# Optimization experiments

Measured on AMD Instinct MI355X. Metric: run time of the kernel, lower is better.

## Reference

```python
import jax, jax.numpy as jnp
import numpy as np

B, C, N = 64, 81, 8732


def setup_inputs() -> dict:
    key = jax.random.key(0)
    k1, k2, k3, k4, k5 = jax.random.split(key, 5)
    ploc = jax.random.normal(k1, (B, 4, N), dtype=jnp.float32)
    plabel = jax.random.normal(k2, (B, C, N), dtype=jnp.float32)
    # gloc: uniform, shifted positive so gwh/dwh log is well-defined
    gloc = jax.random.uniform(k3, (B, 4, N), dtype=jnp.float32) * 0.9 + 0.05
    glabel = jax.random.randint(k4, (B, N), 0, C, dtype=jnp.int64)
    # default boxes: keep widths/heights bounded away from 0
    dboxes = jax.random.uniform(k5, (1, 4, N), dtype=jnp.float32) * 0.9 + 0.1
    return {"ploc": ploc, "plabel": plabel, "gloc": gloc, "glabel": glabel, "dboxes": dboxes}


def _smooth_l1(x):
    ax = jnp.abs(x)
    return jnp.where(ax < 1.0, 0.5 * ax * ax, ax - 0.5)


def reference(ploc, plabel, gloc, glabel, dboxes):
    mask = glabel > 0                       # [B, N] positive anchors
    num_pos = mask.sum(axis=1)              # [B]

    # encode ground-truth boxes as offsets relative to default boxes
    dxy, dwh = dboxes[:, :2, :], dboxes[:, 2:, :]
    gxy = (gloc[:, :2, :] - dxy) / dwh
    gwh = jnp.log(gloc[:, 2:, :] / dwh)
    goff = jnp.concatenate([gxy, gwh], axis=1)  # [B, 4, N]

    # localization loss: smooth L1 summed over coords, masked to positives
    loc = _smooth_l1(ploc - goff).sum(axis=1)   # [B, N]
    loc_loss = (mask * loc).sum(axis=1)         # [B]

    # per-anchor cross entropy
    logp = jax.nn.log_softmax(plabel, axis=1)   # [B, C, N]
    closs = -jnp.take_along_axis(logp, glabel[:, None, :], axis=1)[:, 0, :]  # [B, N]

    # hard negative mining via rank (double argsort, descending)
    con_neg = jnp.where(mask, 0.0, closs)
    con_idx = jnp.argsort(-con_neg, axis=1)
    con_rank = jnp.argsort(con_idx, axis=1)
    neg_num = jnp.minimum(3 * num_pos, N)[:, None]
    neg_mask = con_rank < neg_num
    con_loss = (closs * (mask.astype(jnp.float32) + neg_mask.astype(jnp.float32))).sum(axis=1)

    total = loc_loss + con_loss
    num_mask = (num_pos > 0).astype(jnp.float32)
    npos = jnp.clip(num_pos.astype(jnp.float32), 1e-6)
    return ((total * num_mask) / npos).mean()
```

## Files before the change

kernel.cpp:

```cpp
#include <hip/hip_runtime.h>
#include <math.h>

#define BATCH 64
#define NCLS  81
#define NANCH 8732
#define NG    (NANCH / 4)
#define BLK   256
#define BPB   ((NG + BLK - 1) / BLK)

struct Accum {
    float loc[BATCH];
    float posc[BATCH];
    float negc[BATCH];
    int   cnt[BATCH];
};

__device__ inline float smooth_l1(float d) {
    float a = fabsf(d);
    return (a < 1.f) ? 0.5f * a * a : a - 0.5f;
}

__global__ void k_init(Accum* __restrict__ acc, float* __restrict__ out) {
    unsigned int* w = (unsigned int*)acc;
    w[threadIdx.x] = 0u;
    if (threadIdx.x == 0) out[0] = 0.f;
}

__global__ __launch_bounds__(256) void k_main(
    const float* __restrict__ ploc, const float* __restrict__ plabel,
    const float* __restrict__ gloc, const int* __restrict__ glabel,
    const float* __restrict__ dboxes, Accum* __restrict__ acc)
{
    const int b   = blockIdx.x / BPB;
    const int gid = (blockIdx.x % BPB) * BLK + threadIdx.x;

    float l_loc = 0.f, l_posc = 0.f, l_negc = 0.f;
    int   l_cnt = 0;

    if (gid < NG) {
        const float4* pl4 = (const float4*)(plabel + (size_t)b * NCLS * NANCH);
        const int4*   gp  = (const int4*)(glabel + (size_t)b * NANCH);
        const int4    gi  = gp[gid];
        const int g[4] = {gi.x, gi.y, gi.z, gi.w};

        float m[4], s[4], xg[4];
#pragma unroll
        for (int i = 0; i < 4; ++i) { m[i] = -INFINITY; s[i] = 0.f; xg[i] = 0.f; }

        for (int c = 0; c < NCLS; ++c) {
            float4 xv = pl4[c * NG + gid];
            float x[4] = {xv.x, xv.y, xv.z, xv.w};
#pragma unroll
            for (int i = 0; i < 4; ++i) {
                float nm = fmaxf(m[i], x[i]);
                float e  = __expf(fminf(m[i], x[i]) - nm);
                s[i] = (x[i] > m[i]) ? s[i] * e + 1.f : s[i] + e;
                m[i] = nm;
                if (c == g[i]) xg[i] = x[i];
            }
        }

        const float4* pploc = (const float4*)(ploc + (size_t)b * 4 * NANCH);
        const float4* pgloc = (const float4*)(gloc + (size_t)b * 4 * NANCH);
        const float4* pdb   = (const float4*)dboxes;
        float P[4][4], G[4][4], D[4][4];
#pragma unroll
        for (int ch = 0; ch < 4; ++ch) {
            float4 p = pploc[ch * NG + gid];
            float4 q = pgloc[ch * NG + gid];
            float4 d = pdb[ch * NG + gid];
            P[ch][0]=p.x; P[ch][1]=p.y; P[ch][2]=p.z; P[ch][3]=p.w;
            G[ch][0]=q.x; G[ch][1]=q.y; G[ch][2]=q.z; G[ch][3]=q.w;
            D[ch][0]=d.x; D[ch][1]=d.y; D[ch][2]=d.z; D[ch][3]=d.w;
        }

#pragma unroll
        for (int i = 0; i < 4; ++i) {
            float gx = (G[0][i] - D[0][i]) / D[2][i];
            float gy = (G[1][i] - D[1][i]) / D[3][i];
            float gw = __logf(G[2][i] / D[2][i]);
            float gh = __logf(G[3][i] / D[3][i]);
            float loc_i = smooth_l1(P[0][i] - gx) + smooth_l1(P[1][i] - gy)
                        + smooth_l1(P[2][i] - gw) + smooth_l1(P[3][i] - gh);
            float closs = m[i] + __logf(s[i]) - xg[i];
            bool  mk = g[i] > 0;
            l_loc  += mk ? loc_i : 0.f;
            l_posc += mk ? closs : 0.f;
            l_negc += mk ? 0.f : closs;
            l_cnt  += mk ? 1 : 0;
        }
    }

#pragma unroll
    for (int off = 32; off; off >>= 1) {
        l_loc  += __shfl_down(l_loc, off);
        l_posc += __shfl_down(l_posc, off);
        l_negc += __shfl_down(l_negc, off);
        l_cnt  += __shfl_down(l_cnt, off);
    }
    __shared__ float sl[4], sp[4], sn[4];
    __shared__ int   sc[4];
    const int wave = threadIdx.x >> 6, lane = threadIdx.x & 63;
    if (lane == 0) { sl[wave] = l_loc; sp[wave] = l_posc; sn[wave] = l_negc; sc[wave] = l_cnt; }
    __syncthreads();
    if (threadIdx.x == 0) {
        float a = 0.f, p = 0.f, n = 0.f; int ct = 0;
#pragma unroll
        for (int w = 0; w < 4; ++w) { a += sl[w]; p += sp[w]; n += sn[w]; ct += sc[w]; }
        atomicAdd(&acc->loc[b],  a);
        atomicAdd(&acc->posc[b], p);
        atomicAdd(&acc->negc[b], n);
        atomicAdd(&acc->cnt[b],  ct);
    }
}

__device__ float closs_at(const float* __restrict__ plabel, int b, int n, int g) {
    const float* p = plabel + (size_t)b * NCLS * NANCH + n;
    float m = -INFINITY, s = 0.f, xg = 0.f;
    for (int c = 0; c < NCLS; ++c) {
        float x = p[(size_t)c * NANCH];
        float nm = fmaxf(m, x);
        float e  = __expf(fminf(m, x) - nm);
        s = (x > m) ? s * e + 1.f : s + e;
        m = nm;
        if (c == g) xg = x;
    }
    return m + __logf(s) - xg;
}

__global__ __launch_bounds__(256) void k_finalize(
    const float* __restrict__ plabel, const int* __restrict__ glabel,
    Accum* __restrict__ acc, float* __restrict__ out)
{
    const int b = blockIdx.x;
    const int tid = threadIdx.x;
    const int np = acc->cnt[b];
    if (np == 0) return;

    __shared__ float s_sel;
    __shared__ float rs[4], rc[4];
    __shared__ unsigned int hist[256];
    __shared__ unsigned int s_bucket;
    __shared__ long long s_rnext;

    long long K = 3LL * np; if (K > NANCH) K = NANCH;
    const int nn = NANCH - np;

    if ((long long)nn <= K) {
        long long extra = K - nn;
        if (extra >= np) {
            if (tid == 0) s_sel = acc->negc[b] + acc->posc[b];
        } else {
            if (tid < 64) {
                long long cnt = 0; float sum = 0.f;
                for (int base = 0; base < NANCH; base += 64) {
                    int n = base + tid;
                    int gl = (n < NANCH) ? glabel[(size_t)b * NANCH + n] : 0;
                    bool p = gl > 0;
                    unsigned long long bal = __ballot(p);
                    int r = __popcll(bal & ((1ull << tid) - 1ull));
                    if (p && (cnt + r) < extra) sum += closs_at(plabel, b, n, gl);
                    cnt += (long long)__popcll(bal);
                }
#pragma unroll
                for (int off = 32; off; off >>= 1) sum += __shfl_down(sum, off);
                if (tid == 0) s_sel = acc->negc[b] + sum;
            }
        }
    } else {
        unsigned int prefix = 0;
        long long r = K;
        for (int level = 3; level >= 0; --level) {
            const int shift = level * 8;
            hist[tid] = 0u;
            __syncthreads();
            const unsigned int pmask =
                (level == 3) ? 0u : (0xFFFFFFFFu << ((level + 1) * 8));
            for (int n = tid; n < NANCH; n += 256) {
                int gl = glabel[(size_t)b * NANCH + n];
                float v = (gl > 0) ? 0.f : fmaxf(closs_at(plabel, b, n, gl), 0.f);
                unsigned int bits = __float_as_uint(v);
                if ((bits & pmask) == (prefix & pmask))
                    atomicAdd(&hist[(bits >> shift) & 255u], 1u);
            }
            __syncthreads();
            if (tid == 0) {
                long long acc_c = 0; int bsel = 0;
                for (int i = 255; i >= 0; --i) {
                    if (acc_c + (long long)hist[i] >= r) { bsel = i; break; }
                    acc_c += hist[i];
                }
                s_bucket = (unsigned int)bsel;
                s_rnext  = r - acc_c;
            }
            __syncthreads();
            prefix |= (s_bucket << shift);
            r = s_rnext;
            __syncthreads();
        }
        const float T = __uint_as_float(prefix);
        float lsum = 0.f, lcnt = 0.f;
        for (int n = tid; n < NANCH; n += 256) {
            int gl = glabel[(size_t)b * NANCH + n];
            float v = (gl > 0) ? 0.f : fmaxf(closs_at(plabel, b, n, gl), 0.f);
            if (v > T) { lsum += v; lcnt += 1.f; }
        }
#pragma unroll
        for (int off = 32; off; off >>= 1) {
            lsum += __shfl_down(lsum, off);
            lcnt += __shfl_down(lcnt, off);
        }
        const int wave = tid >> 6, lane = tid & 63;
        if (lane == 0) { rs[wave] = lsum; rc[wave] = lcnt; }
        __syncthreads();
        if (tid == 0) {
            float gsum = 0.f, gcnt = 0.f;
#pragma unroll
            for (int w = 0; w < 4; ++w) { gsum += rs[w]; gcnt += rc[w]; }
            s_sel = gsum + ((float)K - gcnt) * T;
        }
    }

    __syncthreads();
    if (tid == 0) {
        float total = acc->loc[b] + acc->posc[b] + s_sel;
        float npos  = fmaxf((float)np, 1e-6f);
        atomicAdd(out, (total / npos) * (1.0f / BATCH));
    }
}

extern "C" void kernel_launch(void* const* d_in, const int* in_sizes, int n_in,
                              void* d_out, int out_size, void* d_ws, size_t ws_size,
                              hipStream_t stream) {
    const float* ploc   = (const float*)d_in[0];
    const float* plabel = (const float*)d_in[1];
    const float* gloc   = (const float*)d_in[2];
    const int*   glabel = (const int*)d_in[3];
    const float* dboxes = (const float*)d_in[4];
    float* out = (float*)d_out;
    Accum* acc = (Accum*)d_ws;

    hipLaunchKernelGGL(k_init, dim3(1), dim3(256), 0, stream, acc, out);
    hipLaunchKernelGGL(k_main, dim3(BATCH * BPB), dim3(256), 0, stream,
                       ploc, plabel, gloc, glabel, dboxes, acc);
    hipLaunchKernelGGL(k_finalize, dim3(BATCH), dim3(256), 0, stream,
                       plabel, glabel, acc, out);
}
```

Measured before the change: 287.7 us.

## Replace atomics and init kernel with per-block partials and single-block finalize

k_main now writes one float4 partial per block instead of issuing global atomics, which removes the k_init launch. A single-block finalize then sums the partials per batch. The common case, where every negative is selected, is computed directly from those sums, and only batches that need it fall back to the selection paths, processed one after another. This saves a launch and the atomic traffic, but any batch that takes the cold path now runs serially inside one block instead of in 64 parallel blocks.

```diff
diff --git a/kernel.cpp b/kernel.cpp
--- a/kernel.cpp
+++ b/kernel.cpp
@@ -8,28 +8,15 @@
 #define BLK   256
 #define BPB   ((NG + BLK - 1) / BLK)
 
-struct Accum {
-    float loc[BATCH];
-    float posc[BATCH];
-    float negc[BATCH];
-    int   cnt[BATCH];
-};
-
 __device__ inline float smooth_l1(float d) {
     float a = fabsf(d);
     return (a < 1.f) ? 0.5f * a * a : a - 0.5f;
 }
 
-__global__ void k_init(Accum* __restrict__ acc, float* __restrict__ out) {
-    unsigned int* w = (unsigned int*)acc;
-    w[threadIdx.x] = 0u;
-    if (threadIdx.x == 0) out[0] = 0.f;
-}
-
 __global__ __launch_bounds__(256) void k_main(
     const float* __restrict__ ploc, const float* __restrict__ plabel,
     const float* __restrict__ gloc, const int* __restrict__ glabel,
-    const float* __restrict__ dboxes, Accum* __restrict__ acc)
+    const float* __restrict__ dboxes, float4* __restrict__ partials)
 {
     const int b   = blockIdx.x / BPB;
     const int gid = (blockIdx.x % BPB) * BLK + threadIdx.x;
@@ -107,10 +94,7 @@
         float a = 0.f, p = 0.f, n = 0.f; int ct = 0;
 #pragma unroll
         for (int w = 0; w < 4; ++w) { a += sl[w]; p += sp[w]; n += sn[w]; ct += sc[w]; }
-        atomicAdd(&acc->loc[b],  a);
-        atomicAdd(&acc->posc[b], p);
-        atomicAdd(&acc->negc[b], n);
-        atomicAdd(&acc->cnt[b],  ct);
+        partials[blockIdx.x] = make_float4(a, p, n, (float)ct);
     }
 }
 
@@ -128,29 +112,58 @@
     return m + __logf(s) - xg;
 }
 
-__global__ __launch_bounds__(256) void k_finalize(
+__global__ __launch_bounds__(256) void k_fin(
     const float* __restrict__ plabel, const int* __restrict__ glabel,
-    Accum* __restrict__ acc, float* __restrict__ out)
+    const float4* __restrict__ partials, float* __restrict__ out)
 {
-    const int b = blockIdx.x;
     const int tid = threadIdx.x;
-    const int np = acc->cnt[b];
-    if (np == 0) return;
-
-    __shared__ float s_sel;
-    __shared__ float rs[4], rc[4];
+    __shared__ float s_contrib[BATCH];
+    __shared__ float s_loc[BATCH], s_posc[BATCH], s_negc[BATCH];
+    __shared__ int   s_np[BATCH], s_cold[BATCH];
     __shared__ unsigned int hist[256];
     __shared__ unsigned int s_bucket;
     __shared__ long long s_rnext;
-
-    long long K = 3LL * np; if (K > NANCH) K = NANCH;
-    const int nn = NANCH - np;
-
-    if ((long long)nn <= K) {
-        long long extra = K - nn;
-        if (extra >= np) {
-            if (tid == 0) s_sel = acc->negc[b] + acc->posc[b];
-        } else {
+    __shared__ float rs[4], rc[4];
+
+    if (tid < BATCH) {
+        const int b = tid;
+        float loc = 0.f, pc = 0.f, nc = 0.f, cf = 0.f;
+#pragma unroll
+        for (int j = 0; j < BPB; ++j) {
+            float4 v = partials[b * BPB + j];
+            loc += v.x; pc += v.y; nc += v.z; cf += v.w;
+        }
+        const int np = (int)(cf + 0.5f);
+        s_loc[b] = loc; s_posc[b] = pc; s_negc[b] = nc; s_np[b] = np;
+        s_contrib[b] = 0.f;
+        s_cold[b] = 0;
+        if (np > 0) {
+            long long K = 3LL * np; if (K > NANCH) K = NANCH;
+            const int nn = NANCH - np;
+            if ((long long)nn <= K) {
+                long long extra = K - nn;
+                if (extra >= np) {
+                    float total = loc + 2.f * pc + nc;
+                    s_contrib[b] = total / fmaxf((float)np, 1e-6f) * (1.f / BATCH);
+                } else {
+                    s_cold[b] = 1;
+                }
+            } else {
+                s_cold[b] = 2;
+            }
+        }
+    }
+    __syncthreads();
+
+    for (int b = 0; b < BATCH; ++b) {
+        const int mode = s_cold[b];
+        if (mode == 0) continue;
+        const int np = s_np[b];
+        long long K = 3LL * np; if (K > NANCH) K = NANCH;
+        const int nn = NANCH - np;
+
+        if (mode == 1) {
+            long long extra = K - nn;
             if (tid < 64) {
                 long long cnt = 0; float sum = 0.f;
                 for (int base = 0; base < NANCH; base += 64) {
@@ -164,68 +177,75 @@
                 }
 #pragma unroll
                 for (int off = 32; off; off >>= 1) sum += __shfl_down(sum, off);
-                if (tid == 0) s_sel = acc->negc[b] + sum;
-            }
-        }
-    } else {
-        unsigned int prefix = 0;
-        long long r = K;
-        for (int level = 3; level >= 0; --level) {
-            const int shift = level * 8;
-            hist[tid] = 0u;
-            __syncthreads();
-            const unsigned int pmask =
-                (level == 3) ? 0u : (0xFFFFFFFFu << ((level + 1) * 8));
+                if (tid == 0) {
+                    float total = s_loc[b] + s_posc[b] + (s_negc[b] + sum);
+                    s_contrib[b] = total / fmaxf((float)np, 1e-6f) * (1.f / BATCH);
+                }
+            }
+        } else {
+            unsigned int prefix = 0;
+            long long r = K;
+            for (int level = 3; level >= 0; --level) {
+                const int shift = level * 8;
+                hist[tid] = 0u;
+                __syncthreads();
+                const unsigned int pmask =
+                    (level == 3) ? 0u : (0xFFFFFFFFu << ((level + 1) * 8));
+                for (int n = tid; n < NANCH; n += 256) {
+                    int gl = glabel[(size_t)b * NANCH + n];
+                    float v = (gl > 0) ? 0.f : fmaxf(closs_at(plabel, b, n, gl), 0.f);
+                    unsigned int bits = __float_as_uint(v);
+                    if ((bits & pmask) == (prefix & pmask))
+                        atomicAdd(&hist[(bits >> shift) & 255u], 1u);
+                }
+                __syncthreads();
+                if (tid == 0) {
+                    long long acc_c = 0; int bsel = 0;
+                    for (int i = 255; i >= 0; --i) {
+                        if (acc_c + (long long)hist[i] >= r) { bsel = i; break; }
+                        acc_c += hist[i];
+                    }
+                    s_bucket = (unsigned int)bsel;
+                    s_rnext  = r - acc_c;
+                }
+                __syncthreads();
+                prefix |= (s_bucket << shift);
+                r = s_rnext;
+                __syncthreads();
+            }
+            const float T = __uint_as_float(prefix);
+            float lsum = 0.f, lcnt = 0.f;
             for (int n = tid; n < NANCH; n += 256) {
                 int gl = glabel[(size_t)b * NANCH + n];
                 float v = (gl > 0) ? 0.f : fmaxf(closs_at(plabel, b, n, gl), 0.f);
-                unsigned int bits = __float_as_uint(v);
-                if ((bits & pmask) == (prefix & pmask))
-                    atomicAdd(&hist[(bits >> shift) & 255u], 1u);
-            }
+                if (v > T) { lsum += v; lcnt += 1.f; }
+            }
+#pragma unroll
+            for (int off = 32; off; off >>= 1) {
+                lsum += __shfl_down(lsum, off);
+                lcnt += __shfl_down(lcnt, off);
+            }
+            const int wave = tid >> 6, lane = tid & 63;
+            if (lane == 0) { rs[wave] = lsum; rc[wave] = lcnt; }
             __syncthreads();
             if (tid == 0) {
-                long long acc_c = 0; int bsel = 0;
-                for (int i = 255; i >= 0; --i) {
-                    if (acc_c + (long long)hist[i] >= r) { bsel = i; break; }
-                    acc_c += hist[i];
-                }
-                s_bucket = (unsigned int)bsel;
-                s_rnext  = r - acc_c;
-            }
-            __syncthreads();
-            prefix |= (s_bucket << shift);
-            r = s_rnext;
-            __syncthreads();
-        }
-        const float T = __uint_as_float(prefix);
-        float lsum = 0.f, lcnt = 0.f;
-        for (int n = tid; n < NANCH; n += 256) {
-            int gl = glabel[(size_t)b * NANCH + n];
-            float v = (gl > 0) ? 0.f : fmaxf(closs_at(plabel, b, n, gl), 0.f);
-            if (v > T) { lsum += v; lcnt += 1.f; }
-        }
-#pragma unroll
-        for (int off = 32; off; off >>= 1) {
-            lsum += __shfl_down(lsum, off);
-            lcnt += __shfl_down(lcnt, off);
-        }
-        const int wave = tid >> 6, lane = tid & 63;
-        if (lane == 0) { rs[wave] = lsum; rc[wave] = lcnt; }
+                float gsum = 0.f, gcnt = 0.f;
+#pragma unroll
+                for (int w = 0; w < 4; ++w) { gsum += rs[w]; gcnt += rc[w]; }
+                float sel = gsum + ((float)K - gcnt) * T;
+                float total = s_loc[b] + s_posc[b] + sel;
+                s_contrib[b] = total / fmaxf((float)np, 1e-6f) * (1.f / BATCH);
+            }
+        }
         __syncthreads();
-        if (tid == 0) {
-            float gsum = 0.f, gcnt = 0.f;
-#pragma unroll
-            for (int w = 0; w < 4; ++w) { gsum += rs[w]; gcnt += rc[w]; }
-            s_sel = gsum + ((float)K - gcnt) * T;
-        }
-    }
-
+    }
     __syncthreads();
+
     if (tid == 0) {
-        float total = acc->loc[b] + acc->posc[b] + s_sel;
-        float npos  = fmaxf((float)np, 1e-6f);
-        atomicAdd(out, (total / npos) * (1.0f / BATCH));
+        float acc = 0.f;
+#pragma unroll
+        for (int b = 0; b < BATCH; ++b) acc += s_contrib[b];
+        out[0] = acc;
     }
 }
 
@@ -238,11 +258,10 @@
     const int*   glabel = (const int*)d_in[3];
     const float* dboxes = (const float*)d_in[4];
     float* out = (float*)d_out;
-    Accum* acc = (Accum*)d_ws;
-
-    hipLaunchKernelGGL(k_init, dim3(1), dim3(256), 0, stream, acc, out);
+    float4* partials = (float4*)d_ws;
+
     hipLaunchKernelGGL(k_main, dim3(BATCH * BPB), dim3(256), 0, stream,
-                       ploc, plabel, gloc, glabel, dboxes, acc);
-    hipLaunchKernelGGL(k_finalize, dim3(BATCH), dim3(256), 0, stream,
-                       plabel, glabel, acc, out);
-}
+                       ploc, plabel, gloc, glabel, dboxes, partials);
+    hipLaunchKernelGGL(k_fin, dim3(1), dim3(256), 0, stream,
+                       plabel, glabel, partials, out);
+}
```

Result: no change. 290.7 us (+1.0%).
